# Performance work log

Measured on AMD Instinct MI355X. Metric: run time of the kernel, lower is better.

The kernel has to match this reference:

```python
import jax, jax.numpy as jnp
import numpy as np

N_NODES = 50000
N_EDGES = 800000
IN, HID, OUT = 512, 256, 128


def spmm(edge_src, edge_dst, edge_weight, x, n_nodes):
    # y[i] = sum_{e: dst[e]==i} w[e] * x[src[e]]   (sparse adjacency @ x)
    msgs = edge_weight[:, None] * x[edge_src]          # [E, F] gather
    return jax.ops.segment_sum(msgs, edge_dst, num_segments=n_nodes)


def setup_inputs() -> dict:
    key = jax.random.key(0)
    k1, k2, k3, k4, k5, k6 = jax.random.split(key, 6)
    features = jax.random.normal(k1, (N_NODES, IN), dtype=jnp.float32)
    edge_src = jax.random.randint(k2, (N_EDGES,), 0, N_NODES, dtype=jnp.int32)
    edge_dst = jax.random.randint(k3, (N_EDGES,), 0, N_NODES, dtype=jnp.int32)
    edge_weight = jax.random.uniform(k4, (N_EDGES,), dtype=jnp.float32)
    # init like torch: uniform(-stdv, stdv), stdv = 1/sqrt(out_dim)
    s1 = 1.0 / np.sqrt(HID)
    s2 = 1.0 / np.sqrt(OUT)
    W1 = jax.random.uniform(k5, (IN, HID), dtype=jnp.float32, minval=-s1, maxval=s1)
    W2 = jax.random.uniform(k6, (HID, OUT), dtype=jnp.float32, minval=-s2, maxval=s2)
    return {"features": features, "edge_src": edge_src, "edge_dst": edge_dst,
            "edge_weight": edge_weight, "W1": W1, "W2": W2}


def reference(features, edge_src, edge_dst, edge_weight, W1, W2):
    n = features.shape[0]
    # layer 1: dense GEMM -> SpMM -> ReLU
    hidden = jax.nn.relu(spmm(edge_src, edge_dst, edge_weight, features @ W1, n))
    # layer 2: dense GEMM -> SpMM
    out = spmm(edge_src, edge_dst, edge_weight, hidden @ W2, n)
    return out
```

## Files before the change

kernel.cpp:

```cpp
#include <hip/hip_runtime.h>

#define NN 50000
#define NE 800000
#define FIN 512
#define FHID 256
#define FOUT 128
#define MPAD 50048

#define TW1_BLOCKS  512
#define TW2_BLOCKS  128

#define NBKT   196
#define BCAP   5120
#define BSTRIDE 16
#define PA_BLOCKS 392
#define E_CHA    2048

#define PB_BLOCKS 196

using bf16x8 = __attribute__((ext_vector_type(8))) short;
using f32x4  = __attribute__((ext_vector_type(4))) float;
using u16x8  = __attribute__((ext_vector_type(8))) unsigned short;

__device__ __forceinline__ unsigned short f2bf(float f) {
    unsigned int u = __builtin_bit_cast(unsigned int, f);
    unsigned int r = (u + 0x7FFFu + ((u >> 16) & 1u)) >> 16;
    return (unsigned short)r;
}
__device__ __forceinline__ float bf2f(unsigned short u) {
    return __builtin_bit_cast(float, (unsigned int)u << 16);
}
__device__ __forceinline__ void gload_lds16(const void* g, void* l) {
    __builtin_amdgcn_global_load_lds(
        (const __attribute__((address_space(1))) void*)g,
        (__attribute__((address_space(3))) void*)l, 16, 0, 0);
}


__global__ __launch_bounds__(256) void fused_passa_prep_kernel(
    const int* __restrict__ src, const int* __restrict__ dst,
    const float* __restrict__ w, int* __restrict__ bcur, int2* __restrict__ barr,
    const float* __restrict__ W1, unsigned short* __restrict__ W1T,
    const float* __restrict__ W2, unsigned short* __restrict__ W2T) {
    int b = blockIdx.x, tid = threadIdx.x;
    if (b < PA_BLOCKS) {
        __shared__ int hist[NBKT];
        __shared__ int resv[NBKT];
        if (tid < NBKT) hist[tid] = 0;
        __syncthreads();
        int base = b * E_CHA + tid;
        int  d[8];
        bool m[8];
#pragma unroll
        for (int j = 0; j < 8; ++j) {
            int e = base + j * 256;
            m[j] = e < NE;
            d[j] = m[j] ? dst[e] : 0;
        }
#pragma unroll
        for (int j = 0; j < 8; ++j)
            if (m[j]) atomicAdd(&hist[d[j] >> 8], 1);
        __syncthreads();
        if (tid < NBKT) {
            int h = hist[tid];
            resv[tid] = (h > 0) ? atomicAdd(&bcur[tid * BSTRIDE], h) : 0;
            hist[tid] = 0;
        }
        __syncthreads();
        int   s[8];
        float wv[8];
#pragma unroll
        for (int j = 0; j < 8; ++j) {
            int e = base + j * 256;
            s[j]  = m[j] ? src[e] : 0;
            wv[j] = m[j] ? w[e] : 0.f;
        }
#pragma unroll
        for (int j = 0; j < 8; ++j) {
            if (m[j]) {
                int bb = d[j] >> 8;
                int r  = atomicAdd(&hist[bb], 1);
                int pos = resv[bb] + r;
                if (pos < BCAP)
                    barr[(size_t)bb * BCAP + pos] =
                        make_int2(s[j] | ((d[j] & 255) << 16), __float_as_int(wv[j]));
            }
        }
    } else if (b < PA_BLOCKS + TW1_BLOCKS) {
        int t = (b - PA_BLOCKS) * 256 + tid;
        int n = t % FHID, k = t / FHID;
        W1T[(size_t)n * FIN + k] = f2bf(W1[t]);
    } else {
        int t = (b - PA_BLOCKS - TW1_BLOCKS) * 256 + tid;
        int n = t % FOUT, k = t / FOUT;
        W2T[(size_t)n * FHID + k] = f2bf(W2[t]);
    }
}


__global__ __launch_bounds__(256) void gemm1_kernel(const float* __restrict__ X,
                                                    const unsigned short* __restrict__ BT,
                                                    unsigned short* __restrict__ C) {
    __shared__ unsigned short As[64 * 64];
    __shared__ unsigned short Bs[256 * 64];

    const int tid  = threadIdx.x;
    const int lane = tid & 63;
    const int wid  = tid >> 6;
    const int brow = blockIdx.x * 64;
    const int r15   = lane & 15;
    const int khalf = (lane >> 4) * 8;

    const int arow0 = tid >> 3;
    const int arow1 = 32 + (tid >> 3);
    const int acol  = (tid & 7) * 8;
    const int g0 = min(brow + arow0, NN - 1);
    const int g1 = min(brow + arow1, NN - 1);
    const float4* ap0 = (const float4*)(X + (size_t)g0 * FIN + acol);
    const float4* ap1 = (const float4*)(X + (size_t)g1 * FIN + acol);
    const int ab0 = arow0 * 128 + ((acol * 2) ^ ((arow0 & 7) << 4));
    const int ab1 = arow1 * 128 + ((acol * 2) ^ ((arow1 & 7) << 4));

    f32x4 acc[4][4] = {};
    float4 a00 = ap0[0], a01 = ap0[1], a10 = ap1[0], a11 = ap1[1];

#pragma unroll
    for (int k = 0; k < 8; ++k) {
        const int k0 = k * 64;
#pragma unroll
        for (int c = 0; c < 8; ++c) {
            int b   = wid * 8192 + c * 1024 + lane * 16;
            int row = b >> 7;
            int cby = (b & 127) ^ ((row & 7) << 4);
            const char* gb = (const char*)(BT + (size_t)row * FIN + k0) + cby;
            gload_lds16(gb, (char*)Bs + wid * 8192 + c * 1024);
        }
        {
            u16x8 v;
            v[0] = f2bf(a00.x); v[1] = f2bf(a00.y); v[2] = f2bf(a00.z); v[3] = f2bf(a00.w);
            v[4] = f2bf(a01.x); v[5] = f2bf(a01.y); v[6] = f2bf(a01.z); v[7] = f2bf(a01.w);
            *(u16x8*)((char*)As + ab0) = v;
            v[0] = f2bf(a10.x); v[1] = f2bf(a10.y); v[2] = f2bf(a10.z); v[3] = f2bf(a10.w);
            v[4] = f2bf(a11.x); v[5] = f2bf(a11.y); v[6] = f2bf(a11.z); v[7] = f2bf(a11.w);
            *(u16x8*)((char*)As + ab1) = v;
        }
        __syncthreads();

        if (k < 7) {
            int q = (k0 + 64) >> 2;
            a00 = ap0[q]; a01 = ap0[q + 1]; a10 = ap1[q]; a11 = ap1[q + 1];
        }

        bf16x8 bfr[4][2];
#pragma unroll
        for (int n = 0; n < 4; ++n) {
            int row = wid * 64 + n * 16 + r15;
            int rb  = row * 128;
            int sw  = (row & 7) << 4;
#pragma unroll
            for (int ks = 0; ks < 2; ++ks)
                bfr[n][ks] = *(const bf16x8*)((const char*)Bs + rb + (((ks * 32 + khalf) * 2) ^ sw));
        }
#pragma unroll
        for (int m = 0; m < 4; ++m) {
            int row = m * 16 + r15;
            int rb  = row * 128;
            int sw  = (row & 7) << 4;
            bf16x8 af0 = *(const bf16x8*)((const char*)As + rb + (((0 + khalf) * 2) ^ sw));
            bf16x8 af1 = *(const bf16x8*)((const char*)As + rb + (((32 + khalf) * 2) ^ sw));
#pragma unroll
            for (int n = 0; n < 4; ++n) {
                acc[m][n] = __builtin_amdgcn_mfma_f32_16x16x32_bf16(af0, bfr[n][0], acc[m][n], 0, 0, 0);
                acc[m][n] = __builtin_amdgcn_mfma_f32_16x16x32_bf16(af1, bfr[n][1], acc[m][n], 0, 0, 0);
            }
        }
        __syncthreads();
    }

    const int rsub = (lane >> 4) * 4;
#pragma unroll
    for (int m = 0; m < 4; ++m) {
#pragma unroll
        for (int r = 0; r < 4; ++r) {
            int grow = brow + m * 16 + rsub + r;
            if (grow < NN) {
#pragma unroll
                for (int n = 0; n < 4; ++n)
                    C[(size_t)grow * FHID + wid * 64 + n * 16 + r15] = f2bf(acc[m][n][r]);
            }
        }
    }
}


__global__ __launch_bounds__(256) void passb_kernel(const int2* __restrict__ barr,
                                                    const int* __restrict__ bcur,
                                                    int* __restrict__ off,
                                                    int2* __restrict__ csr) {
    __shared__ int sc[256];
    __shared__ int cnt[256];
    __shared__ int pre[256];
    __shared__ int wsum[4];
    int b = blockIdx.x, tid = threadIdx.x, lane = tid & 63, wid = tid >> 6;

    int v = (tid < NBKT) ? min(bcur[tid * BSTRIDE], BCAP) : 0;
    int s = v;
#pragma unroll
    for (int d = 1; d < 64; d <<= 1) {
        int t = __shfl_up(s, d, 64);
        if (lane >= d) s += t;
    }
    if (lane == 63) wsum[wid] = s;
    __syncthreads();
    int wo = 0;
#pragma unroll
    for (int j = 0; j < 4; ++j)
        if (j < wid) wo += wsum[j];
    sc[tid] = wo + s - v;
    if (b == 0 && tid == NBKT - 1) off[NN] = wo + s;
    cnt[tid] = 0;
    __syncthreads();

    int bko_b = sc[b];
    int total = min(bcur[b * BSTRIDE], BCAP);
    const int2* seg = barr + (size_t)b * BCAP;

    for (int k = tid; k < total; k += 256)
        atomicAdd(&cnt[(seg[k].x >> 16) & 255], 1);
    __syncthreads();
    int v2 = cnt[tid];
    int s2 = v2;
#pragma unroll
    for (int d = 1; d < 64; d <<= 1) {
        int t = __shfl_up(s2, d, 64);
        if (lane >= d) s2 += t;
    }
    if (lane == 63) wsum[wid] = s2;
    __syncthreads();
    int wo2 = 0;
#pragma unroll
    for (int j = 0; j < 4; ++j)
        if (j < wid) wo2 += wsum[j];
    int base = bko_b + wo2 + s2 - v2;
    pre[tid] = base;
    int n = b * 256 + tid;
    if (n < NN) off[n] = base;
    cnt[tid] = 0;
    __syncthreads();
    for (int k = tid; k < total; k += 256) {
        int2 pl = seg[k];
        int dlow = (pl.x >> 16) & 255;
        int r = atomicAdd(&cnt[dlow], 1);
        csr[pre[dlow] + r] = make_int2(pl.x & 0xFFFF, pl.y);
    }
}


__global__ __launch_bounds__(256) void gemm2_kernel(const unsigned short* __restrict__ A,
                                                    const unsigned short* __restrict__ BT,
                                                    unsigned short* __restrict__ C) {
    __shared__ unsigned short As[64 * 64];
    __shared__ unsigned short Bs[128 * 64];

    const int tid  = threadIdx.x;
    const int lane = tid & 63;
    const int wid  = tid >> 6;
    const int brow = blockIdx.x * 64;
    const int r15   = lane & 15;
    const int khalf = (lane >> 4) * 8;

    f32x4 acc[4][2] = {};

#pragma unroll
    for (int k = 0; k < 4; ++k) {
        const int k0 = k * 64;
#pragma unroll
        for (int c = 0; c < 4; ++c) {
            int b   = wid * 4096 + c * 1024 + lane * 16;
            int row = b >> 7;
            int cby = (b & 127) ^ ((row & 7) << 4);
            const char* gb = (const char*)(BT + (size_t)row * FHID + k0) + cby;
            gload_lds16(gb, (char*)Bs + wid * 4096 + c * 1024);
        }
#pragma unroll
        for (int c = 0; c < 2; ++c) {
            int b   = wid * 2048 + c * 1024 + lane * 16;
            int row = b >> 7;
            int cby = (b & 127) ^ ((row & 7) << 4);
            const char* ga = (const char*)(A + (size_t)(brow + row) * FHID + k0) + cby;
            gload_lds16(ga, (char*)As + wid * 2048 + c * 1024);
        }
        __syncthreads();

        bf16x8 bfr[2][2];
#pragma unroll
        for (int n = 0; n < 2; ++n) {
            int row = wid * 32 + n * 16 + r15;
            int rb  = row * 128;
            int sw  = (row & 7) << 4;
#pragma unroll
            for (int ks = 0; ks < 2; ++ks)
                bfr[n][ks] = *(const bf16x8*)((const char*)Bs + rb + (((ks * 32 + khalf) * 2) ^ sw));
        }
#pragma unroll
        for (int m = 0; m < 4; ++m) {
            int row = m * 16 + r15;
            int rb  = row * 128;
            int sw  = (row & 7) << 4;
            bf16x8 af0 = *(const bf16x8*)((const char*)As + rb + (((0 + khalf) * 2) ^ sw));
            bf16x8 af1 = *(const bf16x8*)((const char*)As + rb + (((32 + khalf) * 2) ^ sw));
#pragma unroll
            for (int n = 0; n < 2; ++n) {
                acc[m][n] = __builtin_amdgcn_mfma_f32_16x16x32_bf16(af0, bfr[n][0], acc[m][n], 0, 0, 0);
                acc[m][n] = __builtin_amdgcn_mfma_f32_16x16x32_bf16(af1, bfr[n][1], acc[m][n], 0, 0, 0);
            }
        }
        __syncthreads();
    }

    const int rsub = (lane >> 4) * 4;
#pragma unroll
    for (int m = 0; m < 4; ++m) {
#pragma unroll
        for (int r = 0; r < 4; ++r) {
            int grow = brow + m * 16 + rsub + r;
            if (grow < NN) {
#pragma unroll
                for (int n = 0; n < 2; ++n)
                    C[(size_t)grow * FOUT + wid * 32 + n * 16 + r15] = f2bf(acc[m][n][r]);
            }
        }
    }
}


__global__ __launch_bounds__(256) void spmm_pair_kernel(const unsigned short* __restrict__ X,
                                                        const int* __restrict__ off,
                                                        const int2* __restrict__ csr,
                                                        unsigned short* __restrict__ Y) {
    int wave = (int)((blockIdx.x * 256 + threadIdx.x) >> 6);
    int lane = threadIdx.x & 63;
    int half = lane >> 5;
    int hl   = lane & 31;
    int n = wave * 2 + half;
    if (n >= NN) return;
    int e0 = off[n];
    int e1 = off[n + 1];
    const size_t fo = (size_t)hl * 8;

    float acc[8] = {};
    for (int e = e0; e < e1; e += 8) {
        int   ss[8];
        float ww[8];
#pragma unroll
        for (int j = 0; j < 8; ++j) {
            int  ee = e + j;
            bool v  = ee < e1;
            int2 sw = csr[v ? ee : e0];
            ss[j] = sw.x;
            ww[j] = v ? __int_as_float(sw.y) : 0.f;
        }
        u16x8 r[8];
#pragma unroll
        for (int j = 0; j < 8; ++j)
            r[j] = *(const u16x8*)(X + (size_t)ss[j] * FHID + fo);
#pragma unroll
        for (int j = 0; j < 8; ++j)
#pragma unroll
            for (int k = 0; k < 8; ++k)
                acc[k] += ww[j] * bf2f(r[j][k]);
    }
    u16x8 o;
#pragma unroll
    for (int k = 0; k < 8; ++k) o[k] = f2bf(fmaxf(acc[k], 0.f));
    *(u16x8*)(Y + (size_t)n * FHID + fo) = o;
}


__global__ __launch_bounds__(256) void spmm_quad_kernel(const unsigned short* __restrict__ X,
                                                        const int* __restrict__ off,
                                                        const int2* __restrict__ csr,
                                                        float* __restrict__ Y) {
    int wave = (int)((blockIdx.x * 256 + threadIdx.x) >> 6);
    int lane = threadIdx.x & 63;
    int q  = lane >> 4;
    int hl = lane & 15;
    int n = wave * 4 + q;
    if (n >= NN) return;
    int e0 = off[n];
    int e1 = off[n + 1];
    const size_t fo = (size_t)hl * 8;

    float acc[8] = {};
    for (int e = e0; e < e1; e += 8) {
        int   ss[8];
        float ww[8];
#pragma unroll
        for (int j = 0; j < 8; ++j) {
            int  ee = e + j;
            bool v  = ee < e1;
            int2 sw = csr[v ? ee : e0];
            ss[j] = sw.x;
            ww[j] = v ? __int_as_float(sw.y) : 0.f;
        }
        u16x8 r[8];
#pragma unroll
        for (int j = 0; j < 8; ++j)
            r[j] = *(const u16x8*)(X + (size_t)ss[j] * FOUT + fo);
#pragma unroll
        for (int j = 0; j < 8; ++j)
#pragma unroll
            for (int k = 0; k < 8; ++k)
                acc[k] += ww[j] * bf2f(r[j][k]);
    }
    float4 o0 = make_float4(acc[0], acc[1], acc[2], acc[3]);
    float4 o1 = make_float4(acc[4], acc[5], acc[6], acc[7]);
    *(float4*)(Y + (size_t)n * FOUT + fo) = o0;
    *(float4*)(Y + (size_t)n * FOUT + fo + 4) = o1;
}


extern "C" void kernel_launch(void* const* d_in, const int* in_sizes, int n_in,
                              void* d_out, int out_size, void* d_ws, size_t ws_size,
                              hipStream_t stream) {
    const float* features = (const float*)d_in[0];
    const int*   edge_src = (const int*)d_in[1];
    const int*   edge_dst = (const int*)d_in[2];
    const float* edge_w   = (const float*)d_in[3];
    const float* W1       = (const float*)d_in[4];
    const float* W2       = (const float*)d_in[5];
    float* out = (float*)d_out;

    char*  ws  = (char*)d_ws;
    size_t ofs = 0;
    auto carve = [&](size_t bytes) -> void* {
        void* r = ws + ofs;
        ofs = (ofs + bytes + 255) & ~(size_t)255;
        return r;
    };
    int*            off   = (int*)carve((NN + 1) * sizeof(int));
    int*            bcur  = (int*)carve(NBKT * BSTRIDE * sizeof(int));
    int2*           barr  = (int2*)carve((size_t)NBKT * BCAP * sizeof(int2));
    int2*           csr   = (int2*)carve((size_t)NE * sizeof(int2));
    unsigned short* W1T   = (unsigned short*)carve((size_t)FHID * FIN * 2);
    unsigned short* W2T   = (unsigned short*)carve((size_t)FOUT * FHID * 2);
    unsigned short* H0b   = (unsigned short*)carve((size_t)MPAD * FHID * 2);
    unsigned short* Hb    = (unsigned short*)carve((size_t)MPAD * FHID * 2);
    unsigned short* H1b   = H0b;

    hipMemsetAsync(bcur, 0, NBKT * BSTRIDE * sizeof(int), stream);

    fused_passa_prep_kernel<<<PA_BLOCKS + TW1_BLOCKS + TW2_BLOCKS, 256, 0, stream>>>(
        edge_src, edge_dst, edge_w, bcur, barr, W1, W1T, W2, W2T);

    gemm1_kernel<<<MPAD / 64, 256, 0, stream>>>(features, W1T, H0b);

    passb_kernel<<<PB_BLOCKS, 256, 0, stream>>>(barr, bcur, off, csr);

    spmm_pair_kernel<<<6250, 256, 0, stream>>>(H0b, off, csr, Hb);

    gemm2_kernel<<<MPAD / 64, 256, 0, stream>>>(Hb, W2T, H1b);
    spmm_quad_kernel<<<3125, 256, 0, stream>>>(H1b, off, csr, out);
}
```

Measured before the change: 169.5 us.

## Fuse passb with gemm1 and spmm1 with gemm2 through LDS

Merges the CSR-building pass and the first GEMM into one launch by partitioning blocks. The first SpMM (with ReLU) is fused into the second GEMM: each block aggregates 64 rows into a swizzled LDS tile and multiplies it by W2T directly, so the hidden activation never makes a round trip through global memory. This also drops two kernel launches. The costs are lower occupancy from the large LDS buffer, a reduced grid for the SpMM phase with less parallelism to hide gather latency, and W2T fragments read straight from global memory instead of staged through LDS.

```diff
diff --git a/kernel.cpp b/kernel.cpp
--- a/kernel.cpp
+++ b/kernel.cpp
@@ -15,7 +15,6 @@
 #define BSTRIDE 16
 #define PA_BLOCKS 392
 #define E_CHA    2048
-
 #define PB_BLOCKS 196
 
 using bf16x8 = __attribute__((ext_vector_type(8))) short;
@@ -98,16 +97,17 @@
 }
 
 
-__global__ __launch_bounds__(256) void gemm1_kernel(const float* __restrict__ X,
-                                                    const unsigned short* __restrict__ BT,
-                                                    unsigned short* __restrict__ C) {
+__device__ __forceinline__ void gemm1_body(const float* __restrict__ X,
+                                           const unsigned short* __restrict__ BT,
+                                           unsigned short* __restrict__ C,
+                                           int bx) {
     __shared__ unsigned short As[64 * 64];
     __shared__ unsigned short Bs[256 * 64];
 
     const int tid  = threadIdx.x;
     const int lane = tid & 63;
     const int wid  = tid >> 6;
-    const int brow = blockIdx.x * 64;
+    const int brow = bx * 64;
     const int r15   = lane & 15;
     const int khalf = (lane >> 4) * 8;
 
@@ -193,10 +193,10 @@
 }
 
 
-__global__ __launch_bounds__(256) void passb_kernel(const int2* __restrict__ barr,
-                                                    const int* __restrict__ bcur,
-                                                    int* __restrict__ off,
-                                                    int2* __restrict__ csr) {
+__device__ __forceinline__ void passb_body(const int2* __restrict__ barr,
+                                           const int* __restrict__ bcur,
+                                           int* __restrict__ off,
+                                           int2* __restrict__ csr) {
     __shared__ int sc[256];
     __shared__ int cnt[256];
     __shared__ int pre[256];
@@ -256,68 +256,98 @@
 }
 
 
-__global__ __launch_bounds__(256) void gemm2_kernel(const unsigned short* __restrict__ A,
-                                                    const unsigned short* __restrict__ BT,
-                                                    unsigned short* __restrict__ C) {
-    __shared__ unsigned short As[64 * 64];
-    __shared__ unsigned short Bs[128 * 64];
+__global__ __launch_bounds__(256) void fused_passb_gemm1_kernel(
+    const int2* __restrict__ barr, const int* __restrict__ bcur,
+    int* __restrict__ off, int2* __restrict__ csr,
+    const float* __restrict__ X, const unsigned short* __restrict__ BT,
+    unsigned short* __restrict__ C) {
+    if (blockIdx.x < PB_BLOCKS) {
+        passb_body(barr, bcur, off, csr);
+    } else {
+        gemm1_body(X, BT, C, blockIdx.x - PB_BLOCKS);
+    }
+}
+
+
+__global__ __launch_bounds__(256) void fused_spmm1_gemm2_kernel(
+    const unsigned short* __restrict__ H0,
+    const int* __restrict__ off, const int2* __restrict__ csr,
+    const unsigned short* __restrict__ W2T,
+    unsigned short* __restrict__ H1) {
+    __shared__ unsigned short hid[4 * 64 * 64];
 
     const int tid  = threadIdx.x;
     const int lane = tid & 63;
     const int wid  = tid >> 6;
     const int brow = blockIdx.x * 64;
+
+    const int half  = lane >> 5;
+    const int hl    = lane & 31;
+    const int panel = hl >> 3;
+    const int pcolb = (hl & 7) * 16;
+    for (int j = 0; j < 8; ++j) {
+        int row = wid * 16 + j * 2 + half;
+        int n   = brow + row;
+        float acc[8] = {};
+        if (n < NN) {
+            int e0 = off[n], e1 = off[n + 1];
+            for (int e = e0; e < e1; e += 8) {
+                unsigned ssb[8];
+                float    ww[8];
+#pragma unroll
+                for (int q = 0; q < 8; ++q) {
+                    int  ee = e + q;
+                    bool v  = ee < e1;
+                    int2 sw = csr[v ? ee : e0];
+                    ssb[q] = (unsigned)(sw.x * (FHID * 2));
+                    ww[q]  = v ? __int_as_float(sw.y) : 0.f;
+                }
+                u16x8 r[8];
+#pragma unroll
+                for (int q = 0; q < 8; ++q)
+                    r[q] = *(const u16x8*)((const char*)H0 + ssb[q] + hl * 16);
+#pragma unroll
+                for (int q = 0; q < 8; ++q)
+#pragma unroll
+                    for (int kk = 0; kk < 8; ++kk)
+                        acc[kk] += ww[q] * bf2f(r[q][kk]);
+            }
+        }
+        u16x8 o;
+#pragma unroll
+        for (int kk = 0; kk < 8; ++kk) o[kk] = f2bf(fmaxf(acc[kk], 0.f));
+        int byte = panel * 8192 + row * 128 + (pcolb ^ ((row & 7) << 4));
+        *(u16x8*)((char*)hid + byte) = o;
+    }
+    __syncthreads();
+
     const int r15   = lane & 15;
     const int khalf = (lane >> 4) * 8;
-
-    f32x4 acc[4][2] = {};
-
+    f32x4 acc2[4][2] = {};
 #pragma unroll
     for (int k = 0; k < 4; ++k) {
-        const int k0 = k * 64;
-#pragma unroll
-        for (int c = 0; c < 4; ++c) {
-            int b   = wid * 4096 + c * 1024 + lane * 16;
-            int row = b >> 7;
-            int cby = (b & 127) ^ ((row & 7) << 4);
-            const char* gb = (const char*)(BT + (size_t)row * FHID + k0) + cby;
-            gload_lds16(gb, (char*)Bs + wid * 4096 + c * 1024);
-        }
-#pragma unroll
-        for (int c = 0; c < 2; ++c) {
-            int b   = wid * 2048 + c * 1024 + lane * 16;
-            int row = b >> 7;
-            int cby = (b & 127) ^ ((row & 7) << 4);
-            const char* ga = (const char*)(A + (size_t)(brow + row) * FHID + k0) + cby;
-            gload_lds16(ga, (char*)As + wid * 2048 + c * 1024);
-        }
-        __syncthreads();
-
         bf16x8 bfr[2][2];
 #pragma unroll
-        for (int n = 0; n < 2; ++n) {
-            int row = wid * 32 + n * 16 + r15;
-            int rb  = row * 128;
-            int sw  = (row & 7) << 4;
+        for (int n2 = 0; n2 < 2; ++n2) {
+            int wrow = wid * 32 + n2 * 16 + r15;
 #pragma unroll
             for (int ks = 0; ks < 2; ++ks)
-                bfr[n][ks] = *(const bf16x8*)((const char*)Bs + rb + (((ks * 32 + khalf) * 2) ^ sw));
+                bfr[n2][ks] = *(const bf16x8*)(W2T + (size_t)wrow * FHID + k * 64 + ks * 32 + khalf);
         }
 #pragma unroll
         for (int m = 0; m < 4; ++m) {
             int row = m * 16 + r15;
-            int rb  = row * 128;
+            int rb  = k * 8192 + row * 128;
             int sw  = (row & 7) << 4;
-            bf16x8 af0 = *(const bf16x8*)((const char*)As + rb + (((0 + khalf) * 2) ^ sw));
-            bf16x8 af1 = *(const bf16x8*)((const char*)As + rb + (((32 + khalf) * 2) ^ sw));
-#pragma unroll
-            for (int n = 0; n < 2; ++n) {
-                acc[m][n] = __builtin_amdgcn_mfma_f32_16x16x32_bf16(af0, bfr[n][0], acc[m][n], 0, 0, 0);
-                acc[m][n] = __builtin_amdgcn_mfma_f32_16x16x32_bf16(af1, bfr[n][1], acc[m][n], 0, 0, 0);
-            }
-        }
-        __syncthreads();
-    }
-
+            bf16x8 af0 = *(const bf16x8*)((const char*)hid + rb + (((0  + khalf) * 2) ^ sw));
+            bf16x8 af1 = *(const bf16x8*)((const char*)hid + rb + (((32 + khalf) * 2) ^ sw));
+#pragma unroll
+            for (int n2 = 0; n2 < 2; ++n2) {
+                acc2[m][n2] = __builtin_amdgcn_mfma_f32_16x16x32_bf16(af0, bfr[n2][0], acc2[m][n2], 0, 0, 0);
+                acc2[m][n2] = __builtin_amdgcn_mfma_f32_16x16x32_bf16(af1, bfr[n2][1], acc2[m][n2], 0, 0, 0);
+            }
+        }
+    }
     const int rsub = (lane >> 4) * 4;
 #pragma unroll
     for (int m = 0; m < 4; ++m) {
@@ -326,54 +356,11 @@
             int grow = brow + m * 16 + rsub + r;
             if (grow < NN) {
 #pragma unroll
-                for (int n = 0; n < 2; ++n)
-                    C[(size_t)grow * FOUT + wid * 32 + n * 16 + r15] = f2bf(acc[m][n][r]);
-            }
-        }
-    }
-}
-
-
-__global__ __launch_bounds__(256) void spmm_pair_kernel(const unsigned short* __restrict__ X,
-                                                        const int* __restrict__ off,
-                                                        const int2* __restrict__ csr,
-                                                        unsigned short* __restrict__ Y) {
-    int wave = (int)((blockIdx.x * 256 + threadIdx.x) >> 6);
-    int lane = threadIdx.x & 63;
-    int half = lane >> 5;
-    int hl   = lane & 31;
-    int n = wave * 2 + half;
-    if (n >= NN) return;
-    int e0 = off[n];
-    int e1 = off[n + 1];
-    const size_t fo = (size_t)hl * 8;
-
-    float acc[8] = {};
-    for (int e = e0; e < e1; e += 8) {
-        int   ss[8];
-        float ww[8];
-#pragma unroll
-        for (int j = 0; j < 8; ++j) {
-            int  ee = e + j;
-            bool v  = ee < e1;
-            int2 sw = csr[v ? ee : e0];
-            ss[j] = sw.x;
-            ww[j] = v ? __int_as_float(sw.y) : 0.f;
-        }
-        u16x8 r[8];
-#pragma unroll
-        for (int j = 0; j < 8; ++j)
-            r[j] = *(const u16x8*)(X + (size_t)ss[j] * FHID + fo);
-#pragma unroll
-        for (int j = 0; j < 8; ++j)
-#pragma unroll
-            for (int k = 0; k < 8; ++k)
-                acc[k] += ww[j] * bf2f(r[j][k]);
-    }
-    u16x8 o;
-#pragma unroll
-    for (int k = 0; k < 8; ++k) o[k] = f2bf(fmaxf(acc[k], 0.f));
-    *(u16x8*)(Y + (size_t)n * FHID + fo) = o;
+                for (int n2 = 0; n2 < 2; ++n2)
+                    H1[(size_t)grow * FOUT + wid * 32 + n2 * 16 + r15] = f2bf(acc2[m][n2][r]);
+            }
+        }
+    }
 }
 
 
@@ -389,24 +376,23 @@
     if (n >= NN) return;
     int e0 = off[n];
     int e1 = off[n + 1];
-    const size_t fo = (size_t)hl * 8;
 
     float acc[8] = {};
     for (int e = e0; e < e1; e += 8) {
-        int   ss[8];
-        float ww[8];
+        unsigned ssb[8];
+        float    ww[8];
 #pragma unroll
         for (int j = 0; j < 8; ++j) {
             int  ee = e + j;
             bool v  = ee < e1;
             int2 sw = csr[v ? ee : e0];
-            ss[j] = sw.x;
-            ww[j] = v ? __int_as_float(sw.y) : 0.f;
+            ssb[j] = (unsigned)(sw.x * (FOUT * 2));
+            ww[j]  = v ? __int_as_float(sw.y) : 0.f;
         }
         u16x8 r[8];
 #pragma unroll
         for (int j = 0; j < 8; ++j)
-            r[j] = *(const u16x8*)(X + (size_t)ss[j] * FOUT + fo);
+            r[j] = *(const u16x8*)((const char*)X + ssb[j] + hl * 16);
 #pragma unroll
         for (int j = 0; j < 8; ++j)
 #pragma unroll
@@ -415,8 +401,8 @@
     }
     float4 o0 = make_float4(acc[0], acc[1], acc[2], acc[3]);
     float4 o1 = make_float4(acc[4], acc[5], acc[6], acc[7]);
-    *(float4*)(Y + (size_t)n * FOUT + fo) = o0;
-    *(float4*)(Y + (size_t)n * FOUT + fo + 4) = o1;
+    *(float4*)(Y + (size_t)n * FOUT + hl * 8) = o0;
+    *(float4*)(Y + (size_t)n * FOUT + hl * 8 + 4) = o1;
 }
 
 
@@ -445,20 +431,17 @@
     unsigned short* W1T   = (unsigned short*)carve((size_t)FHID * FIN * 2);
     unsigned short* W2T   = (unsigned short*)carve((size_t)FOUT * FHID * 2);
     unsigned short* H0b   = (unsigned short*)carve((size_t)MPAD * FHID * 2);
-    unsigned short* Hb    = (unsigned short*)carve((size_t)MPAD * FHID * 2);
-    unsigned short* H1b   = H0b;
+    unsigned short* H1b   = (unsigned short*)carve((size_t)MPAD * FOUT * 2);
 
     hipMemsetAsync(bcur, 0, NBKT * BSTRIDE * sizeof(int), stream);
 
     fused_passa_prep_kernel<<<PA_BLOCKS + TW1_BLOCKS + TW2_BLOCKS, 256, 0, stream>>>(
         edge_src, edge_dst, edge_w, bcur, barr, W1, W1T, W2, W2T);
 
-    gemm1_kernel<<<MPAD / 64, 256, 0, stream>>>(features, W1T, H0b);
-
-    passb_kernel<<<PB_BLOCKS, 256, 0, stream>>>(barr, bcur, off, csr);
-
-    spmm_pair_kernel<<<6250, 256, 0, stream>>>(H0b, off, csr, Hb);
-
-    gemm2_kernel<<<MPAD / 64, 256, 0, stream>>>(Hb, W2T, H1b);
+    fused_passb_gemm1_kernel<<<PB_BLOCKS + MPAD / 64, 256, 0, stream>>>(
+        barr, bcur, off, csr, features, W1T, H0b);
+
+    fused_spmm1_gemm2_kernel<<<MPAD / 64, 256, 0, stream>>>(H0b, off, csr, W2T, H1b);
+
     spmm_quad_kernel<<<3125, 256, 0, stream>>>(H1b, off, csr, out);
 }
```

New measurement: 173.4 us. 1.02x slower.
